# Kernel optimization log

Measured on AMD Instinct MI355X. Metric: run time of the kernel, lower is better.

The kernel has to match this reference:

```python
import jax, jax.numpy as jnp
import numpy as np

B, N = 32, 512
NFEAT, NHID, NCLASS, NHEADS = 128, 64, 128, 8
WORK_D, SUB_D = 32, 32
H1, H2, OUT_D = 256, 256, 512
ALPHA = 0.2
NEG = -9e15


def setup_inputs() -> dict:
    key = jax.random.key(0)
    ks = jax.random.split(key, 16)
    return {
        "graph_inf": jax.random.normal(ks[0], (B, N, NFEAT), jnp.float32),
        "graph_matrix": jax.random.randint(ks[1], (B, N, N), 0, 2, jnp.int32),
        "masks": jnp.ones((B, N), jnp.float32),
        "node_order": jax.random.randint(ks[2], (B,), 0, N, jnp.int64),
        "work": jax.random.normal(ks[3], (B, WORK_D), jnp.float32),
        "subtask": jax.random.normal(ks[4], (B, SUB_D), jnp.float32),
        # GAT head params
        "W_heads": jax.random.normal(ks[5], (NHEADS, NFEAT, NHID), jnp.float32) * 0.1,
        "a_heads": jax.random.normal(ks[6], (NHEADS, 2 * NHID), jnp.float32) * 0.1,
        "W_out": jax.random.normal(ks[7], (NHID * NHEADS, NCLASS), jnp.float32) * 0.05,
        "a_out": jax.random.normal(ks[8], (2 * NCLASS,), jnp.float32) * 0.1,
        # MLP encoder params
        "fc1_w": jax.random.normal(ks[9], (NCLASS + WORK_D + SUB_D, H1), jnp.float32) * 0.07,
        "fc1_b": jnp.zeros((H1,), jnp.float32),
        "fc2_w": jax.random.normal(ks[10], (H1, H2), jnp.float32) * 0.06,
        "fc2_b": jnp.zeros((H2,), jnp.float32),
        "fc3_w": jax.random.normal(ks[11], (H2, OUT_D), jnp.float32) * 0.06,
        "fc3_b": jnp.zeros((OUT_D,), jnp.float32),
    }


def _gat_layer(Wh, a1, a2, adj, masks):
    # Wh: [B,N,F]; additive GAT score e_ij = leakyrelu(a1.Wh_i + a2.Wh_j)
    s1 = Wh @ a1  # [B,N]
    s2 = Wh @ a2  # [B,N]
    e = jax.nn.leaky_relu(s1[:, :, None] + s2[:, None, :], ALPHA)  # [B,N,N]
    att = jax.nn.softmax(jnp.where(adj > 0, e, NEG), axis=2)
    h_prime = jnp.einsum('bnm,bmf->bnf', att, Wh)
    return h_prime * masks[:, :, None]


def reference(graph_inf, graph_matrix, masks, node_order, work, subtask,
              W_heads, a_heads, W_out, a_out,
              fc1_w, fc1_b, fc2_w, fc2_b, fc3_w, fc3_b):
    adj = graph_matrix
    # multi-head GAT layer (concat=True -> ELU)
    def head(Wk, ak):
        Wh = jnp.einsum('bnf,fo->bno', graph_inf, Wk)
        return jax.nn.elu(_gat_layer(Wh, ak[:NHID], ak[NHID:], adj, masks))
    xh = jax.vmap(head)(W_heads, a_heads)  # [H,B,N,NHID]
    x = jnp.transpose(xh, (1, 2, 0, 3)).reshape(B, N, NHEADS * NHID)
    # output GAT layer (concat=False)
    Wh = jnp.einsum('bnf,fo->bno', x, W_out)
    x = _gat_layer(Wh, a_out[:NCLASS], a_out[NCLASS:], adj, masks)
    x = x * masks[:, :, None]
    # select subtask node per batch element
    selected = x[jnp.arange(B), node_order]  # [B,NCLASS]
    inf = jnp.concatenate([selected, work, subtask], axis=1)
    h = jax.nn.relu(inf @ fc1_w + fc1_b)
    h = jax.nn.relu(h @ fc2_w + fc2_b)
    out = h @ fc3_w + fc3_b
    return jax.nn.softmax(out, axis=-1)
```

## Files before the change

### kernel.cpp

```cpp
#include <hip/hip_runtime.h>

typedef unsigned short u16;
typedef unsigned int u32;
typedef unsigned long long u64;

typedef __bf16 bf16x8 __attribute__((ext_vector_type(8)));
typedef float f32x4 __attribute__((ext_vector_type(4)));

#define LOG2E 1.44269504088896340736f

__device__ __forceinline__ float b2f(u16 u) {
    u32 x = ((u32)u) << 16;
    return __builtin_bit_cast(float, x);
}
__device__ __forceinline__ u16 f2b(float f) {
    u32 u = __builtin_bit_cast(u32, f);
    u32 r = (u + 0x7fffu + ((u >> 16) & 1u)) >> 16;
    return (u16)r;
}
__device__ __forceinline__ float ld(const void* p, int i, bool bf) {
    return bf ? b2f(((const u16*)p)[i]) : ((const float*)p)[i];
}
__device__ __forceinline__ bool detect_bf16(const void* masks) {
    return ((const u16*)masks)[0] != 0;
}
__device__ __forceinline__ f32x4 mfma16(bf16x8 a, bf16x8 b, f32x4 c) {
    return __builtin_amdgcn_mfma_f32_16x16x32_bf16(a, b, c, 0, 0, 0);
}

__device__ __attribute__((aligned(256))) u32  g_adjm[16384 * 16];
__device__ __attribute__((aligned(256))) u16  g_BT1[512 * 128];
__device__ __attribute__((aligned(256))) u16  g_BT2[128 * 512];
__device__ __attribute__((aligned(256))) u16  g_Xc[32 * 512 * 128];
__device__ __attribute__((aligned(256))) u16  g_Wh1[512 * 16384];
__device__ __attribute__((aligned(256))) u16  g_xb[16384 * 512];
__device__ __attribute__((aligned(256))) u16  g_Wh2[16384 * 128];
__device__ __attribute__((aligned(256))) float g_s1a[131072];
__device__ __attribute__((aligned(256))) float g_s2a[131072];
__device__ __attribute__((aligned(256))) float g_s1b[16384];
__device__ __attribute__((aligned(256))) float g_s2b[16384];
__device__ __attribute__((aligned(256))) u16  g_fc1T[256 * 192];
__device__ __attribute__((aligned(256))) u16  g_fc2T[256 * 256];
__device__ __attribute__((aligned(256))) u16  g_fc3T[512 * 256];
__device__ __attribute__((aligned(256))) u16  g_Ahi[32 * 192];
__device__ __attribute__((aligned(256))) u16  g_Alo[32 * 192];

__global__ __launch_bounds__(256) void prep_kernel(
    const int* __restrict__ adj, const void* __restrict__ Whd,
    const void* __restrict__ Wo, const void* __restrict__ Xin,
    const void* __restrict__ fc1w, const void* __restrict__ fc2w,
    const void* __restrict__ fc3w, const void* __restrict__ masks)
{
    const bool bf = detect_bf16(masks);
    const int blk = blockIdx.x;
    const int tid = threadIdx.x;
    if (blk < 1024) {
        int id = blk * 256 + tid;
        int row = id >> 4, w = id & 15;
        const int4* p = (const int4*)(adj + row * 512 + w * 32);
        int4 v[8];
        #pragma unroll
        for (int s = 0; s < 8; ++s) v[s] = p[s];
        u32 word = 0;
        #pragma unroll
        for (int s = 0; s < 8; ++s) {
            u32 nib = (v[s].x > 0 ? 1u : 0u) | (v[s].y > 0 ? 2u : 0u) |
                      (v[s].z > 0 ? 4u : 0u) | (v[s].w > 0 ? 8u : 0u);
            word |= nib << (4 * s);
        }
        g_adjm[id] = word;
    } else if (blk < 1028) {
        int base = (blk - 1024) * 16384;
        for (int e = base + tid; e < base + 16384; e += 256) {
            int n = e >> 7, k = e & 127;
            g_BT1[e] = f2b(ld(Whd, (n >> 6) * 8192 + k * 64 + (n & 63), bf));
        }
    } else if (blk < 1032) {
        int base = (blk - 1028) * 16384;
        for (int e = base + tid; e < base + 16384; e += 256) {
            int n = e >> 9, k = e & 511;
            g_BT2[e] = f2b(ld(Wo, k * 128 + n, bf));
        }
    } else if (blk < 1288) {
        if (!bf) {
            int base = (blk - 1032) * 8192;
            for (int e = base + tid; e < base + 8192; e += 256)
                g_Xc[e] = f2b(((const float*)Xin)[e]);
        }
    } else if (blk < 1294) {
        int base = (blk - 1288) * 8192;
        for (int e = base + tid; e < base + 8192; e += 256) {
            int n = e / 192, k = e - n * 192;
            g_fc1T[e] = f2b(ld(fc1w, k * 256 + n, bf));
        }
    } else if (blk < 1302) {
        int base = (blk - 1294) * 8192;
        for (int e = base + tid; e < base + 8192; e += 256) {
            int n = e >> 8, k = e & 255;
            g_fc2T[e] = f2b(ld(fc2w, k * 256 + n, bf));
        }
    } else {
        int base = (blk - 1302) * 8192;
        for (int e = base + tid; e < base + 8192; e += 256) {
            int n = e >> 8, k = e & 255;
            g_fc3T[e] = f2b(ld(fc3w, k * 512 + n, bf));
        }
    }
}

__global__ __launch_bounds__(256, 2) void gemm1_kernel(
    const void* __restrict__ Xin, const void* __restrict__ a_heads,
    const void* __restrict__ masks)
{
    __shared__ __attribute__((aligned(16))) u16 Asl[128 * 72];
    __shared__ __attribute__((aligned(16))) u16 Bsl[128 * 72];
    const bool bf = detect_bf16(masks);
    const u16* Bsrc = bf ? (const u16*)Xin : g_Xc;
    const int tid = threadIdx.x;
    const int wave = tid >> 6, lane = tid & 63;
    const int wr = wave >> 1, wc = wave & 1;
    const int c = lane & 15, q = lane >> 4;
    const int tm = blockIdx.x * 128, tn = blockIdx.y * 128;
    const int srow = tid >> 1, sh = (tid & 1) * 32;
    f32x4 acc[4][4] = {};
    for (int kc = 0; kc < 128; kc += 64) {
        __syncthreads();
        const u16* Ag = g_BT1 + (tm + srow) * 128 + kc + sh;
        const u16* Bg = Bsrc + (tn + srow) * 128 + kc + sh;
        #pragma unroll
        for (int s = 0; s < 4; ++s) {
            *(uint4*)&Asl[srow * 72 + sh + 8 * s] = *(const uint4*)(Ag + 8 * s);
            *(uint4*)&Bsl[srow * 72 + sh + 8 * s] = *(const uint4*)(Bg + 8 * s);
        }
        __syncthreads();
        #pragma unroll
        for (int kt = 0; kt < 2; ++kt) {
            bf16x8 af[4], bfr[4];
            #pragma unroll
            for (int rt = 0; rt < 4; ++rt)
                af[rt] = *(const bf16x8*)&Asl[(wr * 64 + rt * 16 + c) * 72 + kt * 32 + q * 8];
            #pragma unroll
            for (int ct = 0; ct < 4; ++ct)
                bfr[ct] = *(const bf16x8*)&Bsl[(wc * 64 + ct * 16 + c) * 72 + kt * 32 + q * 8];
            #pragma unroll
            for (int rt = 0; rt < 4; ++rt)
                #pragma unroll
                for (int ct = 0; ct < 4; ++ct)
                    acc[rt][ct] = mfma16(af[rt], bfr[ct], acc[rt][ct]);
        }
    }
    #pragma unroll
    for (int rt = 0; rt < 4; ++rt)
        #pragma unroll
        for (int ct = 0; ct < 4; ++ct)
            #pragma unroll
            for (int i = 0; i < 4; ++i) {
                int r = tm + wr * 64 + rt * 16 + q * 4 + i;
                int col = tn + wc * 64 + ct * 16 + c;
                g_Wh1[r * 16384 + col] = f2b(acc[rt][ct][i]);
            }
    const bool bff = detect_bf16(masks);
    const int hh = blockIdx.x * 2 + wr;
    const int b = tn >> 9;
    const int nbase = (tn & 511) + wc * 64;
    float a1v[4][4], a2v[4][4];
    #pragma unroll
    for (int rt = 0; rt < 4; ++rt)
        #pragma unroll
        for (int i = 0; i < 4; ++i) {
            int o = rt * 16 + q * 4 + i;
            a1v[rt][i] = ld(a_heads, hh * 128 + o, bff);
            a2v[rt][i] = ld(a_heads, hh * 128 + 64 + o, bff);
        }
    #pragma unroll
    for (int ct = 0; ct < 4; ++ct) {
        float p1 = 0.f, p2 = 0.f;
        #pragma unroll
        for (int rt = 0; rt < 4; ++rt)
            #pragma unroll
            for (int i = 0; i < 4; ++i) {
                p1 += acc[rt][ct][i] * a1v[rt][i];
                p2 += acc[rt][ct][i] * a2v[rt][i];
            }
        p1 += __shfl_xor(p1, 16); p1 += __shfl_xor(p1, 32);
        p2 += __shfl_xor(p2, 16); p2 += __shfl_xor(p2, 32);
        if (lane < 16) {
            int n = nbase + ct * 16 + lane;
            g_s1a[(b * 8 + hh) * 512 + n] = p1 * LOG2E;
            g_s2a[(b * 8 + hh) * 512 + n] = p2 * LOG2E;
        }
    }
}

__global__ __launch_bounds__(256, 4) void att1_kernel(const void* __restrict__ masks)
{
    __shared__ float s1s[128];
    __shared__ float s2s[512];

    const bool bf = detect_bf16(masks);
    const int tid = threadIdx.x;
    const int w = tid >> 6, lane = tid & 63;
    const int c = lane & 15, q = lane >> 4;
    const int q4 = blockIdx.x & 3;
    const int h  = (blockIdx.x >> 2) & 7;
    const int b  = blockIdx.x >> 5;

    s2s[tid]       = g_s2a[(b * 8 + h) * 512 + tid];
    s2s[tid + 256] = g_s2a[(b * 8 + h) * 512 + 256 + tid];
    if (tid < 128) s1s[tid] = g_s1a[(b * 8 + h) * 512 + q4 * 128 + tid];
    __syncthreads();

    const u32* adjb = g_adjm + b * 8192;
    const u16* wt = g_Wh1 + (u32)(h * 64) * 16384 + b * 512;

    const u32 bword = (c == 0) ? 0x3F803F80u : 0u;
    const uint4 bq = {bword, bword, bword, bword};
    const bf16x8 bone = __builtin_bit_cast(bf16x8, bq);

    f32x4 acc[2][4] = {};
    f32x4 acc1[2] = {};
    const int row0 = q4 * 128 + w * 16 + c;
    const int row1 = row0 + 64;
    const float s1v0 = s1s[w * 16 + c];
    const float s1v1 = s1s[64 + w * 16 + c];

    for (int kc = 0; kc < 4; ++kc) {
        union { uint4 v; u32 a[4]; } wq0, wq1;
        wq0.v = *(const uint4*)(adjb + row0 * 16 + kc * 4);
        wq1.v = *(const uint4*)(adjb + row1 * 16 + kc * 4);
        #pragma unroll
        for (int tl = 0; tl < 4; ++tl) {
            union { float4 v[2]; float f[8]; } s2r;
            s2r.v[0] = *(const float4*)&s2s[kc * 128 + tl * 32 + q * 8];
            s2r.v[1] = *(const float4*)&s2s[kc * 128 + tl * 32 + q * 8 + 4];
            bf16x8 bfrag[4];
            #pragma unroll
            for (int nt = 0; nt < 4; ++nt)
                bfrag[nt] = *(const bf16x8*)(wt + (u32)(nt * 16 + c) * 16384 +
                                             kc * 128 + tl * 32 + q * 8);
            #pragma unroll
            for (int g = 0; g < 2; ++g) {
                const float s1v = g ? s1v1 : s1v0;
                u32 wbits = (g ? wq1.a[tl] : wq0.a[tl]) >> (q * 8);
                u32 pk[4];
                #pragma unroll
                for (int pi = 0; pi < 4; ++pi) {
                    float e0 = s1v + s2r.f[2 * pi];
                    float e1 = s1v + s2r.f[2 * pi + 1];
                    e0 = fmaxf(e0, 0.2f * e0);
                    e1 = fmaxf(e1, 0.2f * e1);
                    u32 u0 = __builtin_bit_cast(u32, exp2f(e0));
                    u32 u1 = __builtin_bit_cast(u32, exp2f(e1));
                    u0 = ((wbits >> (2 * pi)) & 1u) ? u0 : 0u;
                    u1 = ((wbits >> (2 * pi + 1)) & 1u) ? u1 : 0u;
                    pk[pi] = __builtin_amdgcn_perm(u1, u0, 0x07060302u);
                }
                uint4 pkv = {pk[0], pk[1], pk[2], pk[3]};
                bf16x8 pv = __builtin_bit_cast(bf16x8, pkv);
                acc1[g] = mfma16(pv, bone, acc1[g]);
                #pragma unroll
                for (int nt = 0; nt < 4; ++nt)
                    acc[g][nt] = mfma16(pv, bfrag[nt], acc[g][nt]);
            }
        }
    }
    #pragma unroll
    for (int g = 0; g < 2; ++g) {
        const int R = q4 * 128 + g * 64 + w * 16;
        #pragma unroll
        for (int i = 0; i < 4; ++i) {
            float lr = __shfl(acc1[g][i], (lane & 48));
            float invr = (lr == 0.f) ? (1.f / 512.f) : (1.f / lr);
            const int row = R + q * 4 + i;
            float mk = ld(masks, b * 512 + row, bf);
            #pragma unroll
            for (int nt = 0; nt < 4; ++nt) {
                float v = acc[g][nt][i] * invr * mk;
                float o = v > 0.f ? v : (__expf(v) - 1.f);
                g_xb[(b * 512 + row) * 512 + h * 64 + nt * 16 + c] = f2b(o);
            }
        }
    }
}

__global__ __launch_bounds__(256, 2) void gemm2_kernel(
    const void* __restrict__ a_out, const void* __restrict__ masks)
{
    __shared__ __attribute__((aligned(16))) u16 Asl[64 * 72];
    __shared__ __attribute__((aligned(16))) u16 Bsl[128 * 72];
    const int tid = threadIdx.x;
    const int w = tid >> 6, lane = tid & 63;
    const int c = lane & 15, q = lane >> 4;
    const int tm = blockIdx.x * 64;
    const int rowA = tid >> 2, shA = (tid & 3) * 16;
    const int rowB = tid >> 1, shB = (tid & 1) * 32;
    f32x4 acc[8] = {};
    for (int kc = 0; kc < 512; kc += 64) {
        __syncthreads();
        const u16* Ag = g_xb + (tm + rowA) * 512 + kc + shA;
        *(uint4*)&Asl[rowA * 72 + shA] = *(const uint4*)Ag;
        *(uint4*)&Asl[rowA * 72 + shA + 8] = *(const uint4*)(Ag + 8);
        const u16* Bg = g_BT2 + rowB * 512 + kc + shB;
        #pragma unroll
        for (int s = 0; s < 4; ++s)
            *(uint4*)&Bsl[rowB * 72 + shB + 8 * s] = *(const uint4*)(Bg + 8 * s);
        __syncthreads();
        #pragma unroll
        for (int kt = 0; kt < 2; ++kt) {
            bf16x8 av = *(const bf16x8*)&Asl[(w * 16 + c) * 72 + kt * 32 + q * 8];
            #pragma unroll
            for (int ct = 0; ct < 8; ++ct) {
                bf16x8 bv = *(const bf16x8*)&Bsl[(ct * 16 + c) * 72 + kt * 32 + q * 8];
                acc[ct] = mfma16(av, bv, acc[ct]);
            }
        }
    }
    const bool bf = detect_bf16(masks);
    float a1v[8], a2v[8];
    #pragma unroll
    for (int ct = 0; ct < 8; ++ct) {
        a1v[ct] = ld(a_out, ct * 16 + c, bf);
        a2v[ct] = ld(a_out, 128 + ct * 16 + c, bf);
    }
    #pragma unroll
    for (int i = 0; i < 4; ++i) {
        float p1 = 0.f, p2 = 0.f;
        #pragma unroll
        for (int ct = 0; ct < 8; ++ct) {
            p1 += acc[ct][i] * a1v[ct];
            p2 += acc[ct][i] * a2v[ct];
        }
        #pragma unroll
        for (int off = 1; off < 16; off <<= 1) {
            p1 += __shfl_xor(p1, off);
            p2 += __shfl_xor(p2, off);
        }
        if (c == 0) {
            int m = tm + w * 16 + q * 4 + i;
            g_s1b[m] = p1 * LOG2E;
            g_s2b[m] = p2 * LOG2E;
        }
    }
    #pragma unroll
    for (int ct = 0; ct < 8; ++ct)
        #pragma unroll
        for (int i = 0; i < 4; ++i) {
            int m = tm + w * 16 + q * 4 + i;
            g_Wh2[m * 128 + ct * 16 + c] = f2b(acc[ct][i]);
        }
}

__global__ __launch_bounds__(256) void fin_att(
    const void* __restrict__ masks, const int* __restrict__ node_order,
    const void* __restrict__ workv, const void* __restrict__ subtaskv)
{
    __shared__ float att[512];
    __shared__ float parts[16][128];
    __shared__ float redl[4];

    const bool bf = detect_bf16(masks);
    const int b = blockIdx.x, t = threadIdx.x;
    const int lane = t & 63, wv = t >> 6;
    const int istar = node_order[b];

    const float s1v = g_s1b[b * 512 + istar];
    const u32* arow = g_adjm + (b * 512 + istar) * 16;
    float ssum = 0.f;
    #pragma unroll
    for (int rep = 0; rep < 2; ++rep) {
        int j = t + rep * 256;
        float e = s1v + g_s2b[b * 512 + j];
        e = fmaxf(e, 0.2f * e);
        float ex = ((arow[j >> 5] >> (j & 31)) & 1u) ? exp2f(e) : 0.f;
        att[j] = ex;
        ssum += ex;
    }
    for (int off = 1; off < 64; off <<= 1) ssum += __shfl_xor(ssum, off);
    if (lane == 0) redl[wv] = ssum;
    __syncthreads();
    float tot = redl[0] + redl[1] + redl[2] + redl[3];
    bool uni = (tot == 0.f);
    float inv = uni ? (1.f / 512.f) : (1.f / tot);

    const int og = t & 15, jg = t >> 4;
    float acc[8] = {};
    const u16* base = g_Wh2 + (b * 512 + jg * 32) * 128 + og * 8;
    #pragma unroll 8
    for (int j0 = 0; j0 < 32; ++j0) {
        float wgt = uni ? 1.f : att[jg * 32 + j0];
        union { u16 u[8]; uint4 v; } z;
        z.v = *(const uint4*)(base + j0 * 128);
        #pragma unroll
        for (int i = 0; i < 8; ++i) acc[i] += wgt * b2f(z.u[i]);
    }
    #pragma unroll
    for (int i = 0; i < 8; ++i) parts[jg][og * 8 + i] = acc[i];
    __syncthreads();
    float mk = ld(masks, b * 512 + istar, bf);
    if (t < 128) {
        float s = 0.f;
        #pragma unroll
        for (int jj = 0; jj < 16; ++jj) s += parts[jj][t];
        s *= inv * mk * mk;
        u16 hi = f2b(s);
        g_Ahi[b * 192 + t] = hi;
        g_Alo[b * 192 + t] = f2b(s - b2f(hi));
    } else if (t < 160) {
        g_Ahi[b * 192 + t] = bf ? ((const u16*)workv)[b * 32 + t - 128]
                                : f2b(((const float*)workv)[b * 32 + t - 128]);
        g_Alo[b * 192 + t] = 0;
    } else if (t < 192) {
        g_Ahi[b * 192 + t] = bf ? ((const u16*)subtaskv)[b * 32 + t - 160]
                                : f2b(((const float*)subtaskv)[b * 32 + t - 160]);
        g_Alo[b * 192 + t] = 0;
    }
}

__global__ __launch_bounds__(256) void fin_mlp(
    const void* __restrict__ masks,
    const void* __restrict__ fc1b, const void* __restrict__ fc2b,
    const void* __restrict__ fc3b, void* __restrict__ out)
{
    __shared__ __attribute__((aligned(16))) u16 Ah[32][208];
    __shared__ __attribute__((aligned(16))) u16 Al[32][208];
    __shared__ __attribute__((aligned(16))) u16 Bh[32][272];
    __shared__ __attribute__((aligned(16))) u16 Bl[32][272];
    __shared__ float rtmp[32][4];
    __shared__ float Mf[32], Sf[32];

    const bool bf = detect_bf16(masks);
    const int t = threadIdx.x, wv = t >> 6, lane = t & 63;
    const int c = lane & 15, q = lane >> 4;

    for (int e = t; e < 32 * 192; e += 256) {
        int m = e / 192, k = e - m * 192;
        Ah[m][k] = g_Ahi[e];
        Al[m][k] = g_Alo[e];
    }
    __syncthreads();

    {
        f32x4 acc[2][4] = {};
        for (int kt = 0; kt < 6; ++kt) {
            bf16x8 bw[4], ah[2], al[2];
            #pragma unroll
            for (int nt = 0; nt < 4; ++nt)
                bw[nt] = *(const bf16x8*)&g_fc1T[(wv * 64 + nt * 16 + c) * 192 + kt * 32 + q * 8];
            #pragma unroll
            for (int mt = 0; mt < 2; ++mt) {
                ah[mt] = *(const bf16x8*)&Ah[mt * 16 + c][kt * 32 + q * 8];
                al[mt] = *(const bf16x8*)&Al[mt * 16 + c][kt * 32 + q * 8];
            }
            #pragma unroll
            for (int mt = 0; mt < 2; ++mt)
                #pragma unroll
                for (int nt = 0; nt < 4; ++nt) {
                    acc[mt][nt] = mfma16(ah[mt], bw[nt], acc[mt][nt]);
                    acc[mt][nt] = mfma16(al[mt], bw[nt], acc[mt][nt]);
                }
        }
        #pragma unroll
        for (int mt = 0; mt < 2; ++mt)
            #pragma unroll
            for (int nt = 0; nt < 4; ++nt) {
                int col = wv * 64 + nt * 16 + c;
                float bias = ld(fc1b, col, bf);
                #pragma unroll
                for (int i = 0; i < 4; ++i) {
                    int m = mt * 16 + q * 4 + i;
                    float v = fmaxf(acc[mt][nt][i] + bias, 0.f);
                    u16 hi = f2b(v);
                    Bh[m][col] = hi;
                    Bl[m][col] = f2b(v - b2f(hi));
                }
            }
        __syncthreads();
    }
    {
        f32x4 acc[2][4] = {};
        for (int kt = 0; kt < 8; ++kt) {
            bf16x8 bw[4], ah[2], al[2];
            #pragma unroll
            for (int nt = 0; nt < 4; ++nt)
                bw[nt] = *(const bf16x8*)&g_fc2T[(wv * 64 + nt * 16 + c) * 256 + kt * 32 + q * 8];
            #pragma unroll
            for (int mt = 0; mt < 2; ++mt) {
                ah[mt] = *(const bf16x8*)&Bh[mt * 16 + c][kt * 32 + q * 8];
                al[mt] = *(const bf16x8*)&Bl[mt * 16 + c][kt * 32 + q * 8];
            }
            #pragma unroll
            for (int mt = 0; mt < 2; ++mt)
                #pragma unroll
                for (int nt = 0; nt < 4; ++nt) {
                    acc[mt][nt] = mfma16(ah[mt], bw[nt], acc[mt][nt]);
                    acc[mt][nt] = mfma16(al[mt], bw[nt], acc[mt][nt]);
                }
        }
        __syncthreads();
        #pragma unroll
        for (int mt = 0; mt < 2; ++mt)
            #pragma unroll
            for (int nt = 0; nt < 4; ++nt) {
                int col = wv * 64 + nt * 16 + c;
                float bias = ld(fc2b, col, bf);
                #pragma unroll
                for (int i = 0; i < 4; ++i) {
                    int m = mt * 16 + q * 4 + i;
                    float v = fmaxf(acc[mt][nt][i] + bias, 0.f);
                    u16 hi = f2b(v);
                    Bh[m][col] = hi;
                    Bl[m][col] = f2b(v - b2f(hi));
                }
            }
        __syncthreads();
    }
    f32x4 a3[2][8] = {};
    for (int kt = 0; kt < 8; ++kt) {
        bf16x8 bw[8], ah[2], al[2];
        #pragma unroll
        for (int nt = 0; nt < 8; ++nt)
            bw[nt] = *(const bf16x8*)&g_fc3T[(wv * 128 + nt * 16 + c) * 256 + kt * 32 + q * 8];
        #pragma unroll
        for (int mt = 0; mt < 2; ++mt) {
            ah[mt] = *(const bf16x8*)&Bh[mt * 16 + c][kt * 32 + q * 8];
            al[mt] = *(const bf16x8*)&Bl[mt * 16 + c][kt * 32 + q * 8];
        }
        #pragma unroll
        for (int mt = 0; mt < 2; ++mt)
            #pragma unroll
            for (int nt = 0; nt < 8; ++nt) {
                a3[mt][nt] = mfma16(ah[mt], bw[nt], a3[mt][nt]);
                a3[mt][nt] = mfma16(al[mt], bw[nt], a3[mt][nt]);
            }
    }
    #pragma unroll
    for (int mt = 0; mt < 2; ++mt)
        #pragma unroll
        for (int nt = 0; nt < 8; ++nt) {
            float bias = ld(fc3b, wv * 128 + nt * 16 + c, bf);
            #pragma unroll
            for (int i = 0; i < 4; ++i) a3[mt][nt][i] += bias;
        }
    #pragma unroll
    for (int mt = 0; mt < 2; ++mt)
        #pragma unroll
        for (int i = 0; i < 4; ++i) {
            float mx = a3[mt][0][i];
            #pragma unroll
            for (int nt = 1; nt < 8; ++nt) mx = fmaxf(mx, a3[mt][nt][i]);
            mx = fmaxf(mx, __shfl_xor(mx, 1));
            mx = fmaxf(mx, __shfl_xor(mx, 2));
            mx = fmaxf(mx, __shfl_xor(mx, 4));
            mx = fmaxf(mx, __shfl_xor(mx, 8));
            if (c == 0) rtmp[mt * 16 + q * 4 + i][wv] = mx;
        }
    __syncthreads();
    if (t < 32) Mf[t] = fmaxf(fmaxf(rtmp[t][0], rtmp[t][1]), fmaxf(rtmp[t][2], rtmp[t][3]));
    __syncthreads();
    #pragma unroll
    for (int mt = 0; mt < 2; ++mt)
        #pragma unroll
        for (int i = 0; i < 4; ++i) {
            int row = mt * 16 + q * 4 + i;
            float M = Mf[row];
            float s = 0.f;
            #pragma unroll
            for (int nt = 0; nt < 8; ++nt) s += __expf(a3[mt][nt][i] - M);
            s += __shfl_xor(s, 1);
            s += __shfl_xor(s, 2);
            s += __shfl_xor(s, 4);
            s += __shfl_xor(s, 8);
            if (c == 0) rtmp[row][wv] = s;
        }
    __syncthreads();
    if (t < 32) Sf[t] = 1.f / (rtmp[t][0] + rtmp[t][1] + rtmp[t][2] + rtmp[t][3]);
    __syncthreads();
    #pragma unroll
    for (int mt = 0; mt < 2; ++mt)
        #pragma unroll
        for (int nt = 0; nt < 8; ++nt)
            #pragma unroll
            for (int i = 0; i < 4; ++i) {
                int row = mt * 16 + q * 4 + i;
                int col = wv * 128 + nt * 16 + c;
                float p = __expf(a3[mt][nt][i] - Mf[row]) * Sf[row];
                if (bf) ((u16*)out)[row * 512 + col] = f2b(p);
                else    ((float*)out)[row * 512 + col] = p;
            }
}

extern "C" void kernel_launch(void* const* d_in, const int* in_sizes, int n_in,
                              void* d_out, int out_size, void* d_ws, size_t ws_size,
                              hipStream_t stream)
{
    const void* graph_inf    = d_in[0];
    const int*  graph_matrix = (const int*)d_in[1];
    const void* masks        = d_in[2];
    const int*  node_order   = (const int*)d_in[3];
    const void* work         = d_in[4];
    const void* subtask      = d_in[5];
    const void* W_heads      = d_in[6];
    const void* a_heads      = d_in[7];
    const void* W_out        = d_in[8];
    const void* a_out        = d_in[9];
    const void* fc1w         = d_in[10];
    const void* fc1b         = d_in[11];
    const void* fc2w         = d_in[12];
    const void* fc2b         = d_in[13];
    const void* fc3w         = d_in[14];
    const void* fc3b         = d_in[15];

    prep_kernel<<<dim3(1318), dim3(256), 0, stream>>>(graph_matrix, W_heads, W_out, graph_inf,
                                                      fc1w, fc2w, fc3w, masks);
    gemm1_kernel<<<dim3(4, 128), dim3(256), 0, stream>>>(graph_inf, a_heads, masks);
    att1_kernel<<<dim3(1024), dim3(256), 0, stream>>>(masks);
    gemm2_kernel<<<dim3(256), dim3(256), 0, stream>>>(a_out, masks);
    fin_att<<<dim3(32), dim3(256), 0, stream>>>(masks, node_order, work, subtask);
    fin_mlp<<<dim3(1), dim3(256), 0, stream>>>(masks, fc1b, fc2b, fc3b, d_out);
}
```

Measured before the change: 216.6 us.

## Split single-block MLP tail into multi-block per-layer kernels plus softmax kernel

The final three-layer MLP and output softmax previously ran in one 256-thread block on a single CU. They are now four kernels: each fc layer is spread over 4 or 8 blocks writing hi/lo bf16 activations or fp32 logits to global buffers, followed by a row-wise softmax kernel. The aim is to spread the serial MLP tail across more compute units. In exchange it adds three extra kernel launches and global-memory round trips for the intermediates. It also drops a redundant bf16-detection in gemm1.

```diff
diff --git a/kernel.cpp b/kernel.cpp
--- a/kernel.cpp
+++ b/kernel.cpp
@@ -44,6 +44,11 @@
 __device__ __attribute__((aligned(256))) u16  g_fc3T[512 * 256];
 __device__ __attribute__((aligned(256))) u16  g_Ahi[32 * 192];
 __device__ __attribute__((aligned(256))) u16  g_Alo[32 * 192];
+__device__ __attribute__((aligned(256))) u16  g_H1hi[32 * 256];
+__device__ __attribute__((aligned(256))) u16  g_H1lo[32 * 256];
+__device__ __attribute__((aligned(256))) u16  g_H2hi[32 * 256];
+__device__ __attribute__((aligned(256))) u16  g_H2lo[32 * 256];
+__device__ __attribute__((aligned(256))) float g_logits[32 * 512];
 
 __global__ __launch_bounds__(256) void prep_kernel(
     const int* __restrict__ adj, const void* __restrict__ Whd,
@@ -159,7 +164,6 @@
                 int col = tn + wc * 64 + ct * 16 + c;
                 g_Wh1[r * 16384 + col] = f2b(acc[rt][ct][i]);
             }
-    const bool bff = detect_bf16(masks);
     const int hh = blockIdx.x * 2 + wr;
     const int b = tn >> 9;
     const int nbase = (tn & 511) + wc * 64;
@@ -169,8 +173,8 @@
         #pragma unroll
         for (int i = 0; i < 4; ++i) {
             int o = rt * 16 + q * 4 + i;
-            a1v[rt][i] = ld(a_heads, hh * 128 + o, bff);
-            a2v[rt][i] = ld(a_heads, hh * 128 + 64 + o, bff);
+            a1v[rt][i] = ld(a_heads, hh * 128 + o, bf);
+            a2v[rt][i] = ld(a_heads, hh * 128 + 64 + o, bf);
         }
     #pragma unroll
     for (int ct = 0; ct < 4; ++ct) {
@@ -416,177 +420,93 @@
     }
 }
 
-__global__ __launch_bounds__(256) void fin_mlp(
-    const void* __restrict__ masks,
-    const void* __restrict__ fc1b, const void* __restrict__ fc2b,
-    const void* __restrict__ fc3b, void* __restrict__ out)
-{
-    __shared__ __attribute__((aligned(16))) u16 Ah[32][208];
-    __shared__ __attribute__((aligned(16))) u16 Al[32][208];
-    __shared__ __attribute__((aligned(16))) u16 Bh[32][272];
-    __shared__ __attribute__((aligned(16))) u16 Bl[32][272];
-    __shared__ float rtmp[32][4];
-    __shared__ float Mf[32], Sf[32];
-
-    const bool bf = detect_bf16(masks);
-    const int t = threadIdx.x, wv = t >> 6, lane = t & 63;
+template<int K, int NOUT, bool RELU>
+__device__ __forceinline__ void mlp_body(
+    const u16* __restrict__ Ahi, const u16* __restrict__ Alo,
+    const u16* __restrict__ WT, const void* __restrict__ bias,
+    u16* __restrict__ Ohi, u16* __restrict__ Olo, float* __restrict__ Of,
+    const void* __restrict__ masks)
+{
+    const bool bf = detect_bf16(masks);
+    const int t = threadIdx.x, w = t >> 6, lane = t & 63;
     const int c = lane & 15, q = lane >> 4;
-
-    for (int e = t; e < 32 * 192; e += 256) {
-        int m = e / 192, k = e - m * 192;
-        Ah[m][k] = g_Ahi[e];
-        Al[m][k] = g_Alo[e];
-    }
-    __syncthreads();
-
-    {
-        f32x4 acc[2][4] = {};
-        for (int kt = 0; kt < 6; ++kt) {
-            bf16x8 bw[4], ah[2], al[2];
-            #pragma unroll
-            for (int nt = 0; nt < 4; ++nt)
-                bw[nt] = *(const bf16x8*)&g_fc1T[(wv * 64 + nt * 16 + c) * 192 + kt * 32 + q * 8];
-            #pragma unroll
-            for (int mt = 0; mt < 2; ++mt) {
-                ah[mt] = *(const bf16x8*)&Ah[mt * 16 + c][kt * 32 + q * 8];
-                al[mt] = *(const bf16x8*)&Al[mt * 16 + c][kt * 32 + q * 8];
+    const int col = blockIdx.x * 64 + w * 16 + c;
+
+    const u16* wp  = WT + col * K + q * 8;
+    const u16* ahp = Ahi + c * K + q * 8;
+    const u16* alp = Alo + c * K + q * 8;
+
+    f32x4 acc0 = {}, acc1 = {};
+    #pragma unroll
+    for (int kt = 0; kt < K / 32; ++kt) {
+        bf16x8 bw  = *(const bf16x8*)(wp + kt * 32);
+        bf16x8 ah0 = *(const bf16x8*)(ahp + kt * 32);
+        bf16x8 al0 = *(const bf16x8*)(alp + kt * 32);
+        bf16x8 ah1 = *(const bf16x8*)(ahp + 16 * K + kt * 32);
+        bf16x8 al1 = *(const bf16x8*)(alp + 16 * K + kt * 32);
+        acc0 = mfma16(ah0, bw, acc0);
+        acc0 = mfma16(al0, bw, acc0);
+        acc1 = mfma16(ah1, bw, acc1);
+        acc1 = mfma16(al1, bw, acc1);
+    }
+    float bs = ld(bias, col, bf);
+    #pragma unroll
+    for (int mt = 0; mt < 2; ++mt) {
+        f32x4 a = mt ? acc1 : acc0;
+        #pragma unroll
+        for (int i = 0; i < 4; ++i) {
+            int m = mt * 16 + q * 4 + i;
+            float v = a[i] + bs;
+            if (RELU) {
+                v = fmaxf(v, 0.f);
+                u16 hi = f2b(v);
+                Ohi[m * NOUT + col] = hi;
+                Olo[m * NOUT + col] = f2b(v - b2f(hi));
+            } else {
+                Of[m * NOUT + col] = v;
             }
-            #pragma unroll
-            for (int mt = 0; mt < 2; ++mt)
-                #pragma unroll
-                for (int nt = 0; nt < 4; ++nt) {
-                    acc[mt][nt] = mfma16(ah[mt], bw[nt], acc[mt][nt]);
-                    acc[mt][nt] = mfma16(al[mt], bw[nt], acc[mt][nt]);
-                }
-        }
-        #pragma unroll
-        for (int mt = 0; mt < 2; ++mt)
-            #pragma unroll
-            for (int nt = 0; nt < 4; ++nt) {
-                int col = wv * 64 + nt * 16 + c;
-                float bias = ld(fc1b, col, bf);
-                #pragma unroll
-                for (int i = 0; i < 4; ++i) {
-                    int m = mt * 16 + q * 4 + i;
-                    float v = fmaxf(acc[mt][nt][i] + bias, 0.f);
-                    u16 hi = f2b(v);
-                    Bh[m][col] = hi;
-                    Bl[m][col] = f2b(v - b2f(hi));
-                }
-            }
-        __syncthreads();
-    }
-    {
-        f32x4 acc[2][4] = {};
-        for (int kt = 0; kt < 8; ++kt) {
-            bf16x8 bw[4], ah[2], al[2];
-            #pragma unroll
-            for (int nt = 0; nt < 4; ++nt)
-                bw[nt] = *(const bf16x8*)&g_fc2T[(wv * 64 + nt * 16 + c) * 256 + kt * 32 + q * 8];
-            #pragma unroll
-            for (int mt = 0; mt < 2; ++mt) {
-                ah[mt] = *(const bf16x8*)&Bh[mt * 16 + c][kt * 32 + q * 8];
-                al[mt] = *(const bf16x8*)&Bl[mt * 16 + c][kt * 32 + q * 8];
-            }
-            #pragma unroll
-            for (int mt = 0; mt < 2; ++mt)
-                #pragma unroll
-                for (int nt = 0; nt < 4; ++nt) {
-                    acc[mt][nt] = mfma16(ah[mt], bw[nt], acc[mt][nt]);
-                    acc[mt][nt] = mfma16(al[mt], bw[nt], acc[mt][nt]);
-                }
-        }
-        __syncthreads();
-        #pragma unroll
-        for (int mt = 0; mt < 2; ++mt)
-            #pragma unroll
-            for (int nt = 0; nt < 4; ++nt) {
-                int col = wv * 64 + nt * 16 + c;
-                float bias = ld(fc2b, col, bf);
-                #pragma unroll
-                for (int i = 0; i < 4; ++i) {
-                    int m = mt * 16 + q * 4 + i;
-                    float v = fmaxf(acc[mt][nt][i] + bias, 0.f);
-                    u16 hi = f2b(v);
-                    Bh[m][col] = hi;
-                    Bl[m][col] = f2b(v - b2f(hi));
-                }
-            }
-        __syncthreads();
-    }
-    f32x4 a3[2][8] = {};
-    for (int kt = 0; kt < 8; ++kt) {
-        bf16x8 bw[8], ah[2], al[2];
-        #pragma unroll
-        for (int nt = 0; nt < 8; ++nt)
-            bw[nt] = *(const bf16x8*)&g_fc3T[(wv * 128 + nt * 16 + c) * 256 + kt * 32 + q * 8];
-        #pragma unroll
-        for (int mt = 0; mt < 2; ++mt) {
-            ah[mt] = *(const bf16x8*)&Bh[mt * 16 + c][kt * 32 + q * 8];
-            al[mt] = *(const bf16x8*)&Bl[mt * 16 + c][kt * 32 + q * 8];
-        }
-        #pragma unroll
-        for (int mt = 0; mt < 2; ++mt)
-            #pragma unroll
-            for (int nt = 0; nt < 8; ++nt) {
-                a3[mt][nt] = mfma16(ah[mt], bw[nt], a3[mt][nt]);
-                a3[mt][nt] = mfma16(al[mt], bw[nt], a3[mt][nt]);
-            }
-    }
-    #pragma unroll
-    for (int mt = 0; mt < 2; ++mt)
-        #pragma unroll
-        for (int nt = 0; nt < 8; ++nt) {
-            float bias = ld(fc3b, wv * 128 + nt * 16 + c, bf);
-            #pragma unroll
-            for (int i = 0; i < 4; ++i) a3[mt][nt][i] += bias;
-        }
-    #pragma unroll
-    for (int mt = 0; mt < 2; ++mt)
-        #pragma unroll
-        for (int i = 0; i < 4; ++i) {
-            float mx = a3[mt][0][i];
-            #pragma unroll
-            for (int nt = 1; nt < 8; ++nt) mx = fmaxf(mx, a3[mt][nt][i]);
-            mx = fmaxf(mx, __shfl_xor(mx, 1));
-            mx = fmaxf(mx, __shfl_xor(mx, 2));
-            mx = fmaxf(mx, __shfl_xor(mx, 4));
-            mx = fmaxf(mx, __shfl_xor(mx, 8));
-            if (c == 0) rtmp[mt * 16 + q * 4 + i][wv] = mx;
-        }
-    __syncthreads();
-    if (t < 32) Mf[t] = fmaxf(fmaxf(rtmp[t][0], rtmp[t][1]), fmaxf(rtmp[t][2], rtmp[t][3]));
-    __syncthreads();
-    #pragma unroll
-    for (int mt = 0; mt < 2; ++mt)
-        #pragma unroll
-        for (int i = 0; i < 4; ++i) {
-            int row = mt * 16 + q * 4 + i;
-            float M = Mf[row];
-            float s = 0.f;
-            #pragma unroll
-            for (int nt = 0; nt < 8; ++nt) s += __expf(a3[mt][nt][i] - M);
-            s += __shfl_xor(s, 1);
-            s += __shfl_xor(s, 2);
-            s += __shfl_xor(s, 4);
-            s += __shfl_xor(s, 8);
-            if (c == 0) rtmp[row][wv] = s;
-        }
-    __syncthreads();
-    if (t < 32) Sf[t] = 1.f / (rtmp[t][0] + rtmp[t][1] + rtmp[t][2] + rtmp[t][3]);
-    __syncthreads();
-    #pragma unroll
-    for (int mt = 0; mt < 2; ++mt)
-        #pragma unroll
-        for (int nt = 0; nt < 8; ++nt)
-            #pragma unroll
-            for (int i = 0; i < 4; ++i) {
-                int row = mt * 16 + q * 4 + i;
-                int col = wv * 128 + nt * 16 + c;
-                float p = __expf(a3[mt][nt][i] - Mf[row]) * Sf[row];
-                if (bf) ((u16*)out)[row * 512 + col] = f2b(p);
-                else    ((float*)out)[row * 512 + col] = p;
-            }
+        }
+    }
+}
+
+__global__ __launch_bounds__(256) void mlp1_kernel(const void* bias, const void* masks) {
+    mlp_body<192, 256, true>(g_Ahi, g_Alo, g_fc1T, bias, g_H1hi, g_H1lo, nullptr, masks);
+}
+__global__ __launch_bounds__(256) void mlp2_kernel(const void* bias, const void* masks) {
+    mlp_body<256, 256, true>(g_H1hi, g_H1lo, g_fc2T, bias, g_H2hi, g_H2lo, nullptr, masks);
+}
+__global__ __launch_bounds__(256) void mlp3_kernel(const void* bias, const void* masks) {
+    mlp_body<256, 512, false>(g_H2hi, g_H2lo, g_fc3T, bias, nullptr, nullptr, g_logits, masks);
+}
+
+__global__ __launch_bounds__(64) void softmax_kernel(
+    const void* __restrict__ masks, void* __restrict__ out)
+{
+    const bool bf = detect_bf16(masks);
+    const int row = blockIdx.x, lane = threadIdx.x;
+    const float* lp = g_logits + row * 512 + lane * 8;
+    float v[8];
+    *(float4*)&v[0] = *(const float4*)lp;
+    *(float4*)&v[4] = *(const float4*)(lp + 4);
+    float mx = v[0];
+    #pragma unroll
+    for (int i = 1; i < 8; ++i) mx = fmaxf(mx, v[i]);
+    for (int off = 1; off < 64; off <<= 1) mx = fmaxf(mx, __shfl_xor(mx, off));
+    float e[8];
+    float s = 0.f;
+    #pragma unroll
+    for (int i = 0; i < 8; ++i) { e[i] = __expf(v[i] - mx); s += e[i]; }
+    for (int off = 1; off < 64; off <<= 1) s += __shfl_xor(s, off);
+    float inv = 1.f / s;
+    if (bf) {
+        u16* o = (u16*)out + row * 512 + lane * 8;
+        #pragma unroll
+        for (int i = 0; i < 8; ++i) o[i] = f2b(e[i] * inv);
+    } else {
+        float* o = (float*)out + row * 512 + lane * 8;
+        #pragma unroll
+        for (int i = 0; i < 8; ++i) o[i] = e[i] * inv;
+    }
 }
 
 extern "C" void kernel_launch(void* const* d_in, const int* in_sizes, int n_in,
@@ -616,5 +536,8 @@
     att1_kernel<<<dim3(1024), dim3(256), 0, stream>>>(masks);
     gemm2_kernel<<<dim3(256), dim3(256), 0, stream>>>(a_out, masks);
     fin_att<<<dim3(32), dim3(256), 0, stream>>>(masks, node_order, work, subtask);
-    fin_mlp<<<dim3(1), dim3(256), 0, stream>>>(masks, fc1b, fc2b, fc3b, d_out);
-}
+    mlp1_kernel<<<dim3(4), dim3(256), 0, stream>>>(fc1b, masks);
+    mlp2_kernel<<<dim3(4), dim3(256), 0, stream>>>(fc2b, masks);
+    mlp3_kernel<<<dim3(8), dim3(256), 0, stream>>>(fc3b, masks);
+    softmax_kernel<<<dim3(32), dim3(64), 0, stream>>>(masks, d_out);
+}
```

After: 206.3 us. 4.7% less time.
